# Kernel tuning notes

Measured on AMD Instinct MI355X. Metric: run time of the kernel, lower is better.

Reference implementation:

```python
import jax, jax.numpy as jnp
import numpy as np

N_FFT = 1024
HOP = 256
N_MELS = 128
SR = 16000
EPS = 1e-6
S = 0.025
ALPHA = 0.98
DELTA = 2.0
R = 0.5


def make_mel_fb():
    # Faithful port of F2M._init_buffers (onesided=True)
    n_freq = N_FFT // 2 + 1
    f_max = SR // 2
    m_min = 0.0
    m_max = 2595.0 * np.log10(1.0 + f_max / 700.0)
    m_pts = np.linspace(m_min, m_max, N_MELS + 2)
    f_pts = 700.0 * (10.0 ** (m_pts / 2595.0) - 1.0)
    bins = np.floor((n_freq - 1) * 2 * f_pts / SR).astype(np.int64)
    fb = np.zeros((n_freq, N_MELS), dtype=np.float32)
    for m in range(1, N_MELS + 1):
        a, b, c = int(bins[m - 1]), int(bins[m]), int(bins[m + 1])
        if a != b:
            fb[a:b, m - 1] = (np.arange(a, b) - a) / (b - a)
        if b != c:
            fb[b:c, m - 1] = (c - np.arange(b, c)) / (c - b)
    return jnp.asarray(fb)


def setup_inputs() -> dict:
    key = jax.random.key(0)
    x = jax.random.normal(key, (32, 160000), dtype=jnp.float32)
    return {"x": x, "fb": make_mel_fb()}


def reference(x, fb):
    # torch.stft with center=True (default), rectangular window (window=None)
    pad = N_FFT // 2
    xp = jnp.pad(x, ((0, 0), (pad, pad)), mode="reflect")
    n_frames = (xp.shape[1] - N_FFT) // HOP + 1
    idx = jnp.arange(n_frames)[:, None] * HOP + jnp.arange(N_FFT)[None, :]
    frames = xp[:, idx]                       # [B, T, n_fft]
    spec = jnp.abs(jnp.fft.rfft(frames, axis=-1))   # magnitude, [B, T, F]
    mel = jnp.einsum("btf,fm->btm", spec, fb)       # [B, T, M]

    # PCEN EMA smoother: M_0 = x_0, M_t = (1-s) M_{t-1} + s x_t
    def step(m_prev, frame):
        m = (1.0 - S) * m_prev + S * frame
        return m, m

    x0 = mel[:, 0, :]                               # [B, M]
    _, ms = jax.lax.scan(step, x0, jnp.swapaxes(mel[:, 1:, :], 0, 1))
    M = jnp.concatenate([x0[:, None, :], jnp.swapaxes(ms, 0, 1)], axis=1)

    out = (mel / (M + EPS) ** ALPHA + DELTA) ** R - DELTA ** R
    return out
```

## Files before the change

### kernel.cpp

```cpp
#include <hip/hip_runtime.h>
#include <math.h>

#define NMELS   128
#define NFRAMES 626
#define NPAIRS  313
#define NBATCH  32
#define LSAMP   160000
#define NFREQ   513
#define PPB     4
#define NBLK    ((NPAIRS + PPB - 1) / PPB)
#define NCHUNK  NBLK

struct Bins { int v[NMELS + 2]; };

__device__ __forceinline__ int refl(int i) {
    if (i < 0) i = -i;
    else if (i >= LSAMP) i = 2 * LSAMP - 2 - i;
    return i;
}

__device__ __forceinline__ float2 cadd(float2 a, float2 b){return make_float2(a.x+b.x, a.y+b.y);}
__device__ __forceinline__ float2 csub(float2 a, float2 b){return make_float2(a.x-b.x, a.y-b.y);}
__device__ __forceinline__ float2 cmul(float2 a, float2 b){
    return make_float2(fmaf(a.x,b.x,-a.y*b.y), fmaf(a.x,b.y,a.y*b.x));
}
__device__ __forceinline__ float2 cmulnegi(float2 a){return make_float2(a.y, -a.x);}

__device__ __forceinline__ void dft16(float2* z) {
    const float2 W1 = make_float2( 0.92387953251f, -0.38268343236f);
    const float2 W2 = make_float2( 0.70710678119f, -0.70710678119f);
    const float2 W3 = make_float2( 0.38268343236f, -0.92387953251f);
    const float2 W6 = make_float2(-0.70710678119f, -0.70710678119f);
    const float2 W9 = make_float2(-0.92387953251f,  0.38268343236f);
    float2 g[16];
    #pragma unroll
    for (int q = 0; q < 4; q++) {
        float2 t0=z[q], t1=z[4+q], t2=z[8+q], t3=z[12+q];
        float2 A=cadd(t0,t2), B=csub(t0,t2), C=cadd(t1,t3), D=csub(t1,t3);
        g[q]    = cadd(A,C);
        g[4+q]  = make_float2(B.x + D.y, B.y - D.x);
        g[8+q]  = csub(A,C);
        g[12+q] = make_float2(B.x - D.y, B.y + D.x);
    }
    g[4+1] =cmul(g[4+1], W1); g[4+2] =cmul(g[4+2], W2); g[4+3] =cmul(g[4+3], W3);
    g[8+1] =cmul(g[8+1], W2); g[8+2] =cmulnegi(g[8+2]); g[8+3] =cmul(g[8+3], W6);
    g[12+1]=cmul(g[12+1],W3); g[12+2]=cmul(g[12+2],W6);  g[12+3]=cmul(g[12+3],W9);
    #pragma unroll
    for (int r = 0; r < 4; r++) {
        float2 t0=g[4*r], t1=g[4*r+1], t2=g[4*r+2], t3=g[4*r+3];
        float2 A=cadd(t0,t2), B=csub(t0,t2), C=cadd(t1,t3), D=csub(t1,t3);
        z[r]    = cadd(A,C);
        z[r+4]  = make_float2(B.x + D.y, B.y - D.x);
        z[r+8]  = csub(A,C);
        z[r+12] = make_float2(B.x - D.y, B.y + D.x);
    }
}

__global__ __launch_bounds__(256, 4)
void fft_mel_kernel(const float* __restrict__ x, float* __restrict__ mel,
                    float* __restrict__ S, Bins bins) {
    __shared__ float2 wbuf[PPB][1088];

    const int tid = threadIdx.x;
    const int w   = tid >> 6;
    const int u   = tid & 63;
    const int P   = blockIdx.x;
    const int b   = blockIdx.y;
    const int p   = P * PPB + w;

    float acc[4];

    if (p < NPAIRS) {
        float2* buf  = wbuf[w];
        float*  spec = (float*)&wbuf[w][0];

        const float* xb = x + (size_t)b * LSAMP;
        const int base = 512 * p - 512;
        #pragma unroll
        for (int j = 0; j < 16; j++) {
            const int i = 64 * j + u;
            buf[i] = make_float2(xb[refl(base + i)], xb[refl(base + i + 256)]);
        }

        float2 z[16];

        #pragma unroll
        for (int a = 0; a < 16; a++) z[a] = buf[64*a + u];
        dft16(z);
        {
            float s, c; __sincosf(-(float)M_PI * (float)u * (1.0f/512.0f), &s, &c);
            float2 w1 = make_float2(c, s), wk = w1;
            #pragma unroll
            for (int k = 1; k < 16; k++) { z[k] = cmul(z[k], wk); wk = cmul(wk, w1); }
        }
        #pragma unroll
        for (int k = 0; k < 16; k++) buf[17*u + k] = z[k];

        const int k1 = u >> 2, bp = u & 3;
        #pragma unroll
        for (int a = 0; a < 16; a++) z[a] = buf[68*a + 17*bp + k1];
        dft16(z);
        {
            float s, c; __sincosf(-(float)M_PI * (float)bp * (1.0f/32.0f), &s, &c);
            float2 w1 = make_float2(c, s), wk = w1;
            #pragma unroll
            for (int k = 1; k < 16; k++) { z[k] = cmul(z[k], wk); wk = cmul(wk, w1); }
        }
        #pragma unroll
        for (int k = 0; k < 16; k++) buf[68*k + 17*bp + k1] = z[k];

        #pragma unroll
        for (int j = 0; j < 4; j++) {
            const int c = 64*j + u;
            const int kk1 = c & 15, k2a = c >> 4;
            #pragma unroll
            for (int bq = 0; bq < 4; bq++) z[4*j + bq] = buf[68*k2a + 17*bq + kk1];
        }
        #pragma unroll
        for (int j = 0; j < 4; j++) {
            const int kbase = u + 64*j;
            float2 t0=z[4*j], t1=z[4*j+1], t2=z[4*j+2], t3=z[4*j+3];
            float2 A=cadd(t0,t2), B=csub(t0,t2), C=cadd(t1,t3), D=csub(t1,t3);
            buf[kbase]       = cadd(A,C);
            buf[kbase + 256] = make_float2(B.x + D.y, B.y - D.x);
            buf[kbase + 512] = csub(A,C);
            buf[kbase + 768] = make_float2(B.x - D.y, B.y + D.x);
        }

        float m0[9], m1[9];
        #pragma unroll
        for (int j = 0; j < 9; j++) {
            const int k = 64*j + u;
            if (k <= 512) {
                const int nk = (1024 - k) & 1023;
                float2 Zk = buf[k], Zn = buf[nk];
                float ar = Zk.x + Zn.x, ai = Zk.y - Zn.y;
                float br = Zk.y + Zn.y, bi = Zn.x - Zk.x;
                m0[j] = 0.5f * sqrtf(ar*ar + ai*ai);
                m1[j] = 0.5f * sqrtf(br*br + bi*bi);
            }
        }
        #pragma unroll
        for (int j = 0; j < 9; j++) {
            const int k = 64*j + u;
            if (k <= 512) { spec[k] = m0[j]; spec[NFREQ + k] = m1[j]; }
        }

        const int r = u & 31, pf = u >> 5;
        const float* sp = spec + pf * NFREQ;
        #pragma unroll
        for (int i = 0; i < 4; i++) {
            const int mm = 32*i + r;
            const int a = bins.v[mm], bb = bins.v[mm+1], c = bins.v[mm+2];
            float a0 = 0.f;
            if (bb > a) {
                float s = 0.f;
                for (int f = a; f < bb; f++) s = fmaf(sp[f], (float)(f - a), s);
                a0 += s / (float)(bb - a);
            }
            if (c > bb) {
                float s = 0.f;
                for (int f = bb; f < c; f++) s = fmaf(sp[f], (float)(c - f), s);
                a0 += s / (float)(c - bb);
            }
            acc[i] = a0;
            mel[((size_t)b * NFRAMES + 2*p + pf) * NMELS + mm] = a0;
        }
    }
    __syncthreads();

    float* melst = (float*)&wbuf[0][544];
    if (p < NPAIRS) {
        const int r = u & 31, pf = u >> 5;
        const int fl = 2*w + pf;
        #pragma unroll
        for (int i = 0; i < 4; i++) melst[fl*NMELS + 32*i + r] = acc[i];
    }
    __syncthreads();

    if (tid < NMELS) {
        const int t0 = P * 8;
        const int nf = (NFRAMES - t0 < 8) ? NFRAMES - t0 : 8;
        float s = 0.f;
        for (int f = 0; f < nf; f++) {
            float v = melst[f*NMELS + tid];
            s = (t0 + f == 0) ? v : fmaf(0.975f, s, 0.025f * v);
        }
        S[((size_t)b * NCHUNK + P) * NMELS + tid] = s;
    }
}

__global__ __launch_bounds__(256)
void pcen_scan(const float* __restrict__ S, float* __restrict__ Mstart) {
    const int idx = blockIdx.x * 256 + threadIdx.x;
    const int m = idx & 127;
    const int b = idx >> 7;
    if (b >= NBATCH) return;

    float D8; { float d = 0.975f; d *= d; d *= d; d *= d; D8 = d; }

    const size_t base = (size_t)b * NCHUNK * NMELS + m;
    float M = 0.f;
    #pragma unroll 8
    for (int c = 0; c < NCHUNK; c++) {
        Mstart[base + (size_t)c * NMELS] = M;
        M = fmaf(D8, M, S[base + (size_t)c * NMELS]);
    }
}

__global__ __launch_bounds__(128)
void pcen_out(const float* __restrict__ mel, const float* __restrict__ Mstart,
              float* __restrict__ out) {
    const int m = threadIdx.x;
    const int c = blockIdx.x;
    const int b = blockIdx.y;

    float M = Mstart[((size_t)b * NCHUNK + c) * NMELS + m];

    const int t0 = c * 8;
    const int tend = (t0 + 8 < NFRAMES) ? t0 + 8 : NFRAMES;
    const float* mp = mel + (size_t)b * NFRAMES * NMELS + m;
    float*       op = out + (size_t)b * NFRAMES * NMELS + m;
    #pragma unroll 8
    for (int t = t0; t < tend; t++) {
        float v = mp[(size_t)t * NMELS];
        M = (t == 0) ? v : fmaf(0.975f, M, 0.025f * v);
        float den = __powf(M + 1e-6f, 0.98f);
        op[(size_t)t * NMELS] = sqrtf(v / den + 2.0f) - 1.41421356237f;
    }
}

extern "C" void kernel_launch(void* const* d_in, const int* in_sizes, int n_in,
                              void* d_out, int out_size, void* d_ws, size_t ws_size,
                              hipStream_t stream) {
    const float* x  = (const float*)d_in[0];
    float* out = (float*)d_out;

    float* mel    = (float*)d_ws;
    float* S      = mel + (size_t)NBATCH * NFRAMES * NMELS;
    float* Mstart = S   + (size_t)NBATCH * NCHUNK * NMELS;

    Bins bins;
    {
        const double m_max = 2595.0 * log10(1.0 + 8000.0 / 700.0);
        const double step  = m_max / 129.0;
        for (int i = 0; i < NMELS + 2; i++) {
            double mv = (i == NMELS + 1) ? m_max : (double)i * step;
            double f  = 700.0 * (pow(10.0, mv / 2595.0) - 1.0);
            bins.v[i] = (int)floor((double)(NFREQ - 1) * 2.0 * f / 16000.0);
        }
    }

    dim3 grid1(NBLK, NBATCH);
    fft_mel_kernel<<<grid1, 256, 0, stream>>>(x, mel, S, bins);

    pcen_scan<<<(NBATCH * NMELS + 255) / 256, 256, 0, stream>>>(S, Mstart);

    dim3 grid3(NCHUNK, NBATCH);
    pcen_out<<<grid3, 128, 0, stream>>>(mel, Mstart, out);
}
```

Measured before the change: 123.1 us.

## Vectorize interior frame loads and fold chunk scan into PCEN output kernel

Interior frame pairs now load the contiguous 1280-sample window with float4 reads into shared memory instead of per-element reflected scalar loads, and only the boundary pairs keep the reflect path. The separate pcen_scan kernel is removed; each pcen_out block recomputes its starting smoother state by serially folding the chunk summaries that precede it. This removes a kernel launch and the Mstart round-trip through memory, at the cost of redundant prefix work that grows linearly with the chunk index (up to ~78 dependent loads per thread).

```diff
diff --git a/kernel.cpp b/kernel.cpp
--- a/kernel.cpp
+++ b/kernel.cpp
@@ -72,20 +72,32 @@
 
     if (p < NPAIRS) {
         float2* buf  = wbuf[w];
+        float*  raw  = (float*)&wbuf[w][0];
         float*  spec = (float*)&wbuf[w][0];
 
         const float* xb = x + (size_t)b * LSAMP;
         const int base = 512 * p - 512;
-        #pragma unroll
-        for (int j = 0; j < 16; j++) {
-            const int i = 64 * j + u;
-            buf[i] = make_float2(xb[refl(base + i)], xb[refl(base + i + 256)]);
+        if (p != 0 && p != NPAIRS - 1) {
+            const float* xs = xb + base;
+            #pragma unroll
+            for (int j = 0; j < 5; j++) {
+                const int i = 256 * j + 4 * u;
+                float4 v = *reinterpret_cast<const float4*>(xs + i);
+                *reinterpret_cast<float4*>(raw + i) = v;
+            }
+        } else {
+            #pragma unroll
+            for (int j = 0; j < 20; j++) {
+                const int i = 64 * j + u;
+                raw[i] = xb[refl(base + i)];
+            }
         }
 
         float2 z[16];
 
         #pragma unroll
-        for (int a = 0; a < 16; a++) z[a] = buf[64*a + u];
+        for (int a = 0; a < 16; a++)
+            z[a] = make_float2(raw[64*a + u], raw[64*a + u + 256]);
         dft16(z);
         {
             float s, c; __sincosf(-(float)M_PI * (float)u * (1.0f/512.0f), &s, &c);
@@ -190,32 +202,18 @@
     }
 }
 
-__global__ __launch_bounds__(256)
-void pcen_scan(const float* __restrict__ S, float* __restrict__ Mstart) {
-    const int idx = blockIdx.x * 256 + threadIdx.x;
-    const int m = idx & 127;
-    const int b = idx >> 7;
-    if (b >= NBATCH) return;
-
-    float D8; { float d = 0.975f; d *= d; d *= d; d *= d; D8 = d; }
-
-    const size_t base = (size_t)b * NCHUNK * NMELS + m;
-    float M = 0.f;
-    #pragma unroll 8
-    for (int c = 0; c < NCHUNK; c++) {
-        Mstart[base + (size_t)c * NMELS] = M;
-        M = fmaf(D8, M, S[base + (size_t)c * NMELS]);
-    }
-}
-
 __global__ __launch_bounds__(128)
-void pcen_out(const float* __restrict__ mel, const float* __restrict__ Mstart,
+void pcen_out(const float* __restrict__ mel, const float* __restrict__ S,
               float* __restrict__ out) {
     const int m = threadIdx.x;
     const int c = blockIdx.x;
     const int b = blockIdx.y;
 
-    float M = Mstart[((size_t)b * NCHUNK + c) * NMELS + m];
+    float D8; { float d = 0.975f; d *= d; d *= d; d *= d; D8 = d; }
+
+    const float* Sp = S + (size_t)b * NCHUNK * NMELS + m;
+    float M = 0.f;
+    for (int j = 0; j < c; j++) M = fmaf(D8, M, Sp[(size_t)j * NMELS]);
 
     const int t0 = c * 8;
     const int tend = (t0 + 8 < NFRAMES) ? t0 + 8 : NFRAMES;
@@ -236,9 +234,8 @@
     const float* x  = (const float*)d_in[0];
     float* out = (float*)d_out;
 
-    float* mel    = (float*)d_ws;
-    float* S      = mel + (size_t)NBATCH * NFRAMES * NMELS;
-    float* Mstart = S   + (size_t)NBATCH * NCHUNK * NMELS;
+    float* mel = (float*)d_ws;
+    float* S   = mel + (size_t)NBATCH * NFRAMES * NMELS;
 
     Bins bins;
     {
@@ -254,8 +251,6 @@
     dim3 grid1(NBLK, NBATCH);
     fft_mel_kernel<<<grid1, 256, 0, stream>>>(x, mel, S, bins);
 
-    pcen_scan<<<(NBATCH * NMELS + 255) / 256, 256, 0, stream>>>(S, Mstart);
-
-    dim3 grid3(NCHUNK, NBATCH);
-    pcen_out<<<grid3, 128, 0, stream>>>(mel, Mstart, out);
-}
+    dim3 grid2(NCHUNK, NBATCH);
+    pcen_out<<<grid2, 128, 0, stream>>>(mel, S, out);
+}
```

Result: slower. 127.5 us (+3.5%).
